# Kernel tuning notes

Hardware: AMD Instinct MI355X
Metric: run time of the kernel (lower is better)

## Reference

```python
import jax, jax.numpy as jnp
import numpy as np

N = 50000
E = 800000
DES, TW, NUMP, CATP = 768, 768, 4, 3
EMB = 384
THIRD = EMB // 3  # 128


def _lin(key, fan_in, fan_out):
    k1, k2 = jax.random.split(key)
    bound = 1.0 / np.sqrt(fan_in)
    W = jax.random.uniform(k1, (fan_in, fan_out), jnp.float32, -bound, bound)
    b = jax.random.uniform(k2, (fan_out,), jnp.float32, -bound, bound)
    return W, b


def setup_inputs() -> dict:
    key = jax.random.key(0)
    ks = jax.random.split(key, 16)
    des = jax.random.normal(ks[0], (N, DES), jnp.float32)
    tweet = jax.random.normal(ks[1], (N, TW), jnp.float32)
    num_prop = jax.random.normal(ks[2], (N, NUMP), jnp.float32)
    cat_prop = jax.random.normal(ks[3], (N, CATP), jnp.float32)
    edge_index = jax.random.randint(ks[4], (2, E), 0, N, jnp.int64)
    W_des, b_des = _lin(ks[5], DES, THIRD)
    W_num, b_num = _lin(ks[6], NUMP, THIRD)
    W_cat, b_cat = _lin(ks[7], CATP, THIRD)
    W_in, b_in = _lin(ks[8], EMB, EMB)
    W_g1, b_g1 = _lin(ks[9], EMB, EMB)
    W_g2, b_g2 = _lin(ks[10], EMB, EMB)
    W_o1, b_o1 = _lin(ks[11], EMB, EMB)
    W_o2, b_o2 = _lin(ks[12], EMB, 2)
    return dict(des=des, tweet=tweet, num_prop=num_prop, cat_prop=cat_prop,
                edge_index=edge_index,
                W_des=W_des, b_des=b_des, W_num=W_num, b_num=b_num,
                W_cat=W_cat, b_cat=b_cat, W_in=W_in, b_in=b_in,
                W_g1=W_g1, b_g1=b_g1, W_g2=W_g2, b_g2=b_g2,
                W_o1=W_o1, b_o1=b_o1, W_o2=W_o2, b_o2=b_o2)


def _leaky(x):
    return jax.nn.leaky_relu(x, 0.01)


def _gcn_conv(x, edge_index, W, b):
    # PyG GCNConv: x' = D^{-1/2} (A + I) D^{-1/2} (x W) + b
    src, dst = edge_index[0], edge_index[1]
    x = x @ W  # [N, out]
    n = x.shape[0]
    deg = jax.ops.segment_sum(jnp.ones(src.shape[0], x.dtype), dst, num_segments=n) + 1.0  # self-loop
    dinv = jax.lax.rsqrt(deg)  # deg >= 1
    norm = dinv[src] * dinv[dst]  # [E]
    msg = x[src] * norm[:, None]  # [E, out] gather
    agg = jax.ops.segment_sum(msg, dst, num_segments=n)  # scatter-add
    agg = agg + x * (dinv * dinv)[:, None]  # self-loop contribution
    return agg + b


def reference(des, tweet, num_prop, cat_prop, edge_index,
              W_des, b_des, W_num, b_num, W_cat, b_cat, W_in, b_in,
              W_g1, b_g1, W_g2, b_g2, W_o1, b_o1, W_o2, b_o2):
    # eval mode: dropout is identity
    d = _leaky(des @ W_des + b_des)
    n = _leaky(num_prop @ W_num + b_num)
    c = _leaky(cat_prop @ W_cat + b_cat)
    x = jnp.concatenate((d, n, c), axis=1)  # [N, EMB]
    x = _leaky(x @ W_in + b_in)
    x = _gcn_conv(x, edge_index, W_g1, b_g1)
    x = _gcn_conv(x, edge_index, W_g2, b_g2)
    x = _leaky(x @ W_o1 + b_o1)
    return x @ W_o2 + b_o2  # [N, 2]
```

## Files before the change

### kernel.cpp

```cpp
#include <hip/hip_runtime.h>
#include <hip/hip_bf16.h>
#include <cstdint>

#define NFEAT 384
#define DESK 768
#define THIRD 128

typedef __bf16 bf16x8 __attribute__((ext_vector_type(8)));
typedef unsigned short u16x8 __attribute__((ext_vector_type(8)));
typedef unsigned short u16x4 __attribute__((ext_vector_type(4)));
typedef float f32x16 __attribute__((ext_vector_type(16)));
typedef _Float16 h16x2 __attribute__((ext_vector_type(2)));

__device__ __forceinline__ float leaky(float x) { return x > 0.f ? x : 0.01f * x; }

__device__ __forceinline__ unsigned short bfhi(float x) {
  unsigned int u = __float_as_uint(x);
  u += 0x7fffu + ((u >> 16) & 1u);
  return (unsigned short)(u >> 16);
}
__device__ __forceinline__ float bf2f(unsigned short h) {
  return __uint_as_float(((unsigned int)h) << 16);
}
__device__ __forceinline__ void bsplit(float x, unsigned short& h,
                                       unsigned short& l) {
  h = bfhi(x);
  l = bfhi(x - bf2f(h));
}

__device__ __forceinline__ int swz(int kb, int row, int ROWS) {
  return (kb * ROWS + (row ^ (kb << 1))) * 8;
}

#define MFMA(a, b, c) __builtin_amdgcn_mfma_f32_32x32x16_bf16(a, b, c, 0, 0, 0)

template <int AFP32, int EPI, int BM, int DBUF>
__global__ __launch_bounds__(256, 2) void mfma_gemm(
    const float* __restrict__ Af, const unsigned short* __restrict__ Ahi,
    const unsigned short* __restrict__ Alo,
    const unsigned short* __restrict__ BThi,
    const unsigned short* __restrict__ BTlo, _Float16* __restrict__ Ch16,
    unsigned short* __restrict__ Chi, unsigned short* __restrict__ Clo,
    const float* __restrict__ bias, int M, int K, int ldc) {
  __shared__ unsigned short AhiL[DBUF + 1][4 * BM * 8];
  __shared__ unsigned short AloL[DBUF + 1][4 * BM * 8];
  __shared__ unsigned short BhiL[DBUF + 1][4 * 128 * 8];
  __shared__ unsigned short BloL[DBUF + 1][4 * 128 * 8];
  const int tid = threadIdx.x;
  const int lane = tid & 63;
  const int w = tid >> 6;
  constexpr int MR = BM / 64;
  const int wm = (w >> 1) * (BM / 2);
  const int wn = (w & 1) * 64;
  const int lm = lane & 31, lk = lane >> 5;

  int bx = blockIdx.x, by = blockIdx.y;
  if (gridDim.y == 3) {
    int lin = by * gridDim.x + bx;
    int ng = gridDim.x >> 3;
    int full = ng * 24;
    if (lin < full) {
      int g = lin / 24, x = lin - g * 24;
      bx = g * 8 + (x & 7);
      by = x >> 3;
    } else {
      int rem = lin - full;
      int mrem = gridDim.x - (ng << 3);
      bx = (ng << 3) + rem % mrem;
      by = rem / mrem;
    }
  }
  const int m_base = bx * BM, n_base = by * 128;

  f32x16 acc[MR][2];
#pragma unroll
  for (int mi = 0; mi < MR; mi++)
#pragma unroll
    for (int nt = 0; nt < 2; nt++)
#pragma unroll
      for (int r = 0; r < 16; r++) acc[mi][nt][r] = 0.f;

  constexpr int AIT_F = BM / 32;
  constexpr int AIT_H = BM / 64;
  float4 pa[3][AIT_F];
  u16x8 pah[3][AIT_H], pal[3][AIT_H];
  u16x8 pbh[3][2], pbl[3][2];

  auto loadA = [&](int kt, int s) {
    if (AFP32) {
#pragma unroll
      for (int it = 0; it < AIT_F; it++) {
        int r = (tid >> 3) + it * 32;
        int gr = m_base + r;
        float4 av = make_float4(0.f, 0.f, 0.f, 0.f);
        if (gr < M) av = *(const float4*)&Af[(size_t)gr * K + kt + (tid & 7) * 4];
        pa[s][it] = av;
      }
    } else {
#pragma unroll
      for (int it = 0; it < AIT_H; it++) {
        int r = (tid >> 2) + it * 64;
        int gr = m_base + r;
        u16x8 vh = {0, 0, 0, 0, 0, 0, 0, 0};
        u16x8 vl = {0, 0, 0, 0, 0, 0, 0, 0};
        if (gr < M) {
          vh = *(const u16x8*)&Ahi[(size_t)gr * K + kt + (tid & 3) * 8];
          vl = *(const u16x8*)&Alo[(size_t)gr * K + kt + (tid & 3) * 8];
        }
        pah[s][it] = vh;
        pal[s][it] = vl;
      }
    }
  };
  auto loadB = [&](int kt, int s) {
#pragma unroll
    for (int it = 0; it < 2; it++) {
      int n = (tid >> 2) + it * 64;
      pbh[s][it] = *(const u16x8*)&BThi[(size_t)(n_base + n) * K + kt + (tid & 3) * 8];
      pbl[s][it] = *(const u16x8*)&BTlo[(size_t)(n_base + n) * K + kt + (tid & 3) * 8];
    }
  };
  auto storeLDS = [&](int s, int b) {
    if (AFP32) {
#pragma unroll
      for (int it = 0; it < AIT_F; it++) {
        int r = (tid >> 3) + it * 32;
        int q = tid & 7;
        float4 av = pa[s][it];
        unsigned short h0, h1, h2, h3, l0, l1, l2, l3;
        bsplit(av.x, h0, l0);
        bsplit(av.y, h1, l1);
        bsplit(av.z, h2, l2);
        bsplit(av.w, h3, l3);
        int base = swz(q >> 1, r, BM) + (q & 1) * 4;
        u16x4 th;
        th.x = h0; th.y = h1; th.z = h2; th.w = h3;
        u16x4 tl;
        tl.x = l0; tl.y = l1; tl.z = l2; tl.w = l3;
        *(u16x4*)&AhiL[b][base] = th;
        *(u16x4*)&AloL[b][base] = tl;
      }
    } else {
#pragma unroll
      for (int it = 0; it < AIT_H; it++) {
        int r = (tid >> 2) + it * 64;
        int kb = tid & 3;
        *(u16x8*)&AhiL[b][swz(kb, r, BM)] = pah[s][it];
        *(u16x8*)&AloL[b][swz(kb, r, BM)] = pal[s][it];
      }
    }
#pragma unroll
    for (int it = 0; it < 2; it++) {
      int n = (tid >> 2) + it * 64;
      int kb = tid & 3;
      *(u16x8*)&BhiL[b][swz(kb, n, 128)] = pbh[s][it];
      *(u16x8*)&BloL[b][swz(kb, n, 128)] = pbl[s][it];
    }
  };
  auto compute = [&](int b) {
#pragma unroll
    for (int ks = 0; ks < 2; ks++) {
      int kb = 2 * ks + lk;
      bf16x8 ah[MR], al[MR];
#pragma unroll
      for (int mi = 0; mi < MR; mi++) {
        ah[mi] = __builtin_bit_cast(
            bf16x8, *(const u16x8*)&AhiL[b][swz(kb, wm + mi * 32 + lm, BM)]);
        al[mi] = __builtin_bit_cast(
            bf16x8, *(const u16x8*)&AloL[b][swz(kb, wm + mi * 32 + lm, BM)]);
      }
      bf16x8 bh0 = __builtin_bit_cast(
          bf16x8, *(const u16x8*)&BhiL[b][swz(kb, wn + lm, 128)]);
      bf16x8 bh1 = __builtin_bit_cast(
          bf16x8, *(const u16x8*)&BhiL[b][swz(kb, wn + 32 + lm, 128)]);
      bf16x8 bl0 = __builtin_bit_cast(
          bf16x8, *(const u16x8*)&BloL[b][swz(kb, wn + lm, 128)]);
      bf16x8 bl1 = __builtin_bit_cast(
          bf16x8, *(const u16x8*)&BloL[b][swz(kb, wn + 32 + lm, 128)]);
#pragma unroll
      for (int mi = 0; mi < MR; mi++) {
        acc[mi][0] = MFMA(ah[mi], bh0, acc[mi][0]);
        acc[mi][1] = MFMA(ah[mi], bh1, acc[mi][1]);
        acc[mi][0] = MFMA(ah[mi], bl0, acc[mi][0]);
        acc[mi][1] = MFMA(ah[mi], bl1, acc[mi][1]);
        acc[mi][0] = MFMA(al[mi], bh0, acc[mi][0]);
        acc[mi][1] = MFMA(al[mi], bh1, acc[mi][1]);
      }
    }
  };

  const int NK = K >> 5;
  loadA(0, 0);
  loadB(0, 0);
  loadA(32, 1);
  loadB(32, 1);
  loadA(64, 2);
  loadB(64, 2);

  if (DBUF) {
    storeLDS(0, 0);
    __syncthreads();
    for (int m6 = 0; m6 < NK / 6; m6++) {
#pragma unroll
      for (int ph = 0; ph < 6; ph++) {
        const int i = m6 * 6 + ph;
        if (i + 1 < NK) storeLDS((ph + 1) % 3, (ph + 1) & 1);
        if (i + 3 < NK) {
          loadA((i + 3) << 5, ph % 3);
          loadB((i + 3) << 5, ph % 3);
        }
        compute(ph & 1);
        __syncthreads();
      }
    }
  } else {
    for (int m3 = 0; m3 < NK / 3; m3++) {
#pragma unroll
      for (int ph = 0; ph < 3; ph++) {
        const int i = m3 * 3 + ph;
        storeLDS(ph, 0);
        __syncthreads();
        if (i + 3 < NK) {
          loadA((i + 3) << 5, ph);
          loadB((i + 3) << 5, ph);
        }
        compute(0);
        __syncthreads();
      }
    }
  }

  const int colb = n_base + wn;
#pragma unroll
  for (int mi = 0; mi < MR; mi++) {
#pragma unroll
    for (int nt = 0; nt < 2; nt++) {
      f32x16 v = acc[mi][nt];
      int col = colb + nt * 32 + lm;
      float bv = (EPI == 0) ? bias[col] : 0.f;
      int rb = m_base + wm + mi * 32 + 4 * lk;
#pragma unroll
      for (int rg = 0; rg < 16; rg++) {
        int row = rb + (rg & 3) + 8 * (rg >> 2);
        if (row < M) {
          float x = v[rg];
          if (EPI == 0) {
            x = leaky(x + bv);
            unsigned short h, l;
            bsplit(x, h, l);
            Chi[(size_t)row * ldc + col] = h;
            Clo[(size_t)row * ldc + col] = l;
          } else {
            Ch16[(size_t)row * ldc + col] = (_Float16)x;
          }
        }
      }
    }
  }
}

__global__ __launch_bounds__(256) void split_transpose_b(
    const float* __restrict__ s0, unsigned short* __restrict__ h0,
    unsigned short* __restrict__ l0, const float* __restrict__ s1,
    unsigned short* __restrict__ h1, unsigned short* __restrict__ l1,
    const float* __restrict__ s2, unsigned short* __restrict__ h2,
    unsigned short* __restrict__ l2) {
  int z = blockIdx.z;
  const float* src = z == 0 ? s0 : (z == 1 ? s1 : s2);
  unsigned short* dsthi = z == 0 ? h0 : (z == 1 ? h1 : h2);
  unsigned short* dstlo = z == 0 ? l0 : (z == 1 ? l1 : l2);
  int R = z == 0 ? 768 : 384;
  int C = z == 0 ? 128 : 384;
  int c0 = blockIdx.x * 32, r0 = blockIdx.y * 32;
  if (c0 >= C || r0 >= R) return;
  __shared__ float tile[32][33];
  int tx = threadIdx.x & 31, ty = threadIdx.x >> 5;
#pragma unroll
  for (int i = 0; i < 4; i++)
    tile[ty + i * 8][tx] = src[(size_t)(r0 + ty + i * 8) * C + c0 + tx];
  __syncthreads();
#pragma unroll
  for (int i = 0; i < 4; i++) {
    int c = c0 + ty + i * 8, r = r0 + tx;
    float v = tile[tx][ty + i * 8];
    unsigned short h, l;
    bsplit(v, h, l);
    dsthi[(size_t)c * R + r] = h;
    dstlo[(size_t)c * R + r] = l;
  }
}

__global__ __launch_bounds__(256) void gemm384(const float* __restrict__ A,
                                               const float* __restrict__ B,
                                               float* __restrict__ C) {
  __shared__ float As[16][68];
  __shared__ float Bs[16][64];
  const int tid = threadIdx.x;
  const int mb = blockIdx.x * 64;
  const int nb = blockIdx.y * 64;
  float acc[4][4] = {};
  const int arow = tid >> 2, akq = tid & 3;
  const int brow = tid >> 4, bc4 = tid & 15;
  const int m0 = (tid >> 4) * 4, n0 = (tid & 15) * 4;
  for (int kk = 0; kk < 384; kk += 16) {
    float4 av = *(const float4*)&A[(mb + arow) * 384 + kk + akq * 4];
    As[akq * 4 + 0][arow] = av.x;
    As[akq * 4 + 1][arow] = av.y;
    As[akq * 4 + 2][arow] = av.z;
    As[akq * 4 + 3][arow] = av.w;
    *(float4*)&Bs[brow][bc4 * 4] =
        *(const float4*)&B[(kk + brow) * 384 + nb + bc4 * 4];
    __syncthreads();
#pragma unroll
    for (int k = 0; k < 16; k++) {
      float4 a4 = *(const float4*)&As[k][m0];
      float4 b4 = *(const float4*)&Bs[k][n0];
      float a[4] = {a4.x, a4.y, a4.z, a4.w};
      float b[4] = {b4.x, b4.y, b4.z, b4.w};
#pragma unroll
      for (int i = 0; i < 4; i++)
#pragma unroll
        for (int j = 0; j < 4; j++) acc[i][j] = fmaf(a[i], b[j], acc[i][j]);
    }
    __syncthreads();
  }
#pragma unroll
  for (int i = 0; i < 4; i++)
#pragma unroll
    for (int j = 0; j < 4; j++)
      C[(mb + m0 + i) * 384 + nb + n0 + j] = acc[i][j];
}

__global__ void uv_kernel(const float* __restrict__ T1,
                          const float* __restrict__ W_o1,
                          const float* __restrict__ b_g1,
                          const float* __restrict__ b_g2,
                          const float* __restrict__ b_o1, float* __restrict__ u,
                          float* __restrict__ v) {
  int j = blockIdx.x * blockDim.x + threadIdx.x;
  if (j < 384) {
    float su = 0.f, sv = 0.f;
    for (int k = 0; k < 384; k++) {
      su = fmaf(T1[k * 384 + j], b_g1[k], su);
      sv = fmaf(W_o1[k * 384 + j], b_g2[k], sv);
    }
    u[j] = su;
    v[j] = sv + b_o1[j];
  }
}

__global__ __launch_bounds__(256) void numcat_kernel(
    const float* __restrict__ num, const float* __restrict__ cat,
    const float* __restrict__ Wn, const float* __restrict__ bn,
    const float* __restrict__ Wc, const float* __restrict__ bc,
    unsigned short* __restrict__ x0hi, unsigned short* __restrict__ x0lo,
    int N) {
  int c = threadIdx.x;
  for (int i = blockIdx.x; i < N; i += gridDim.x) {
    float val;
    if (c < 128) {
      val = bn[c];
      val = fmaf(num[i * 4 + 0], Wn[0 * 128 + c], val);
      val = fmaf(num[i * 4 + 1], Wn[1 * 128 + c], val);
      val = fmaf(num[i * 4 + 2], Wn[2 * 128 + c], val);
      val = fmaf(num[i * 4 + 3], Wn[3 * 128 + c], val);
    } else {
      int cc = c - 128;
      val = bc[cc];
      val = fmaf(cat[i * 3 + 0], Wc[0 * 128 + cc], val);
      val = fmaf(cat[i * 3 + 1], Wc[1 * 128 + cc], val);
      val = fmaf(cat[i * 3 + 2], Wc[2 * 128 + cc], val);
    }
    val = leaky(val);
    unsigned short h, l;
    bsplit(val, h, l);
    size_t o = (size_t)i * NFEAT + 128 + c;
    x0hi[o] = h;
    x0lo[o] = l;
  }
}

__global__ void count_kernel(const int* __restrict__ dst, int* __restrict__ deg,
                             int E) {
  int e = blockIdx.x * blockDim.x + threadIdx.x;
  if (e < E) atomicAdd(&deg[dst[e]], 1);
}

__global__ void scan_reduce(const int* __restrict__ deg,
                            int* __restrict__ partial, int N) {
  __shared__ int sm[512];
  int i = blockIdx.x * 512 + threadIdx.x;
  sm[threadIdx.x] = (i < N) ? deg[i] : 0;
  __syncthreads();
  for (int off = 256; off; off >>= 1) {
    if (threadIdx.x < off) sm[threadIdx.x] += sm[threadIdx.x + off];
    __syncthreads();
  }
  if (threadIdx.x == 0) partial[blockIdx.x] = sm[0];
}

__global__ void scan_top(int* partial, int nb) {
  if (threadIdx.x == 0 && blockIdx.x == 0) {
    int run = 0;
    for (int b = 0; b < nb; b++) {
      int t = partial[b];
      partial[b] = run;
      run += t;
    }
  }
}

__global__ void scan_down(const int* __restrict__ deg,
                          const int* __restrict__ partial,
                          int* __restrict__ offsets, int* __restrict__ cursor,
                          float* __restrict__ dinv, int N, int E) {
  __shared__ int sm[512];
  int t = threadIdx.x;
  int i = blockIdx.x * 512 + t;
  int val = (i < N) ? deg[i] : 0;
  sm[t] = val;
  __syncthreads();
  for (int off = 1; off < 512; off <<= 1) {
    int add = (t >= off) ? sm[t - off] : 0;
    __syncthreads();
    sm[t] += add;
    __syncthreads();
  }
  if (i < N) {
    int ex = partial[blockIdx.x] + sm[t] - val;
    offsets[i] = ex;
    cursor[i] = ex;
    dinv[i] = 1.0f / sqrtf((float)val + 1.0f);
  }
  if (i == 0) offsets[N] = E;
}

__global__ void fill_kernel(const int* __restrict__ src,
                            const int* __restrict__ dst,
                            int* __restrict__ cursor,
                            int* __restrict__ csr_off,
                            float* __restrict__ csr_w,
                            const float* __restrict__ dinv, int E) {
  int e = blockIdx.x * blockDim.x + threadIdx.x;
  if (e < E) {
    int s = src[e], d = dst[e];
    int slot = atomicAdd(&cursor[d], 1);
    csr_off[slot] = s * NFEAT;
    csr_w[slot] = dinv[s] * dinv[d];
  }
}

template <int WRITE_S, int FINAL>
__global__ __launch_bounds__(192) void agg_kernel(
    const _Float16* __restrict__ xin, _Float16* __restrict__ xout,
    const int* __restrict__ offsets, const int* __restrict__ csr_off,
    const float* __restrict__ csr_w, const float* __restrict__ dinv,
    float* __restrict__ sout, const float* __restrict__ svec,
    const float* __restrict__ uvec, const float* __restrict__ vvec,
    const float* __restrict__ W_o2, const float* __restrict__ b_o2,
    float* __restrict__ out, int N) {
  const int t = threadIdx.x;
  const int ff = 2 * t;
  __shared__ int ssrc[192];
  __shared__ float sw[192];
  __shared__ float red[3][2];
  float u0 = 0.f, u1 = 0.f, vc0 = 0.f, vc1 = 0.f;
  float w00 = 0.f, w01 = 0.f, w10 = 0.f, w11 = 0.f, bo0 = 0.f, bo1 = 0.f;
  if (FINAL) {
    u0 = uvec[ff];
    u1 = uvec[ff + 1];
    vc0 = vvec[ff];
    vc1 = vvec[ff + 1];
    w00 = W_o2[ff * 2 + 0];
    w01 = W_o2[ff * 2 + 1];
    w10 = W_o2[(ff + 1) * 2 + 0];
    w11 = W_o2[(ff + 1) * 2 + 1];
    bo0 = b_o2[0];
    bo1 = b_o2[1];
  }
  for (int i = blockIdx.x; i < N; i += gridDim.x) {
    int beg = offsets[i], end = offsets[i + 1];
    float di = dinv[i];
    float dii = di * di;
    h16x2 xs = *(const h16x2*)&xin[(size_t)i * NFEAT + ff];
    float A0x = dii * (float)xs.x, A0y = dii * (float)xs.y;
    float A1x = 0.f, A1y = 0.f, A2x = 0.f, A2y = 0.f, A3x = 0.f, A3y = 0.f;
    float wsum = dii;
    for (int j0 = beg; j0 < end; j0 += 192) {
      int cnt = min(192, end - j0);
      if (t < cnt) {
        ssrc[t] = csr_off[j0 + t];
        sw[t] = csr_w[j0 + t];
      }
      __syncthreads();
      int j = 0;
      for (; j + 8 <= cnt; j += 8) {
        int o0 = ssrc[j + 0], o1 = ssrc[j + 1], o2 = ssrc[j + 2],
            o3 = ssrc[j + 3];
        int o4 = ssrc[j + 4], o5 = ssrc[j + 5], o6 = ssrc[j + 6],
            o7 = ssrc[j + 7];
        float w0 = sw[j + 0], w1 = sw[j + 1], w2 = sw[j + 2], w3 = sw[j + 3];
        float w4 = sw[j + 4], w5 = sw[j + 5], w6 = sw[j + 6], w7 = sw[j + 7];
        h16x2 v0 = *(const h16x2*)&xin[o0 + ff];
        h16x2 v1 = *(const h16x2*)&xin[o1 + ff];
        h16x2 v2 = *(const h16x2*)&xin[o2 + ff];
        h16x2 v3 = *(const h16x2*)&xin[o3 + ff];
        h16x2 v4 = *(const h16x2*)&xin[o4 + ff];
        h16x2 v5 = *(const h16x2*)&xin[o5 + ff];
        h16x2 v6 = *(const h16x2*)&xin[o6 + ff];
        h16x2 v7 = *(const h16x2*)&xin[o7 + ff];
        A0x = fmaf(w0, (float)v0.x, A0x);
        A0y = fmaf(w0, (float)v0.y, A0y);
        A1x = fmaf(w1, (float)v1.x, A1x);
        A1y = fmaf(w1, (float)v1.y, A1y);
        A2x = fmaf(w2, (float)v2.x, A2x);
        A2y = fmaf(w2, (float)v2.y, A2y);
        A3x = fmaf(w3, (float)v3.x, A3x);
        A3y = fmaf(w3, (float)v3.y, A3y);
        A0x = fmaf(w4, (float)v4.x, A0x);
        A0y = fmaf(w4, (float)v4.y, A0y);
        A1x = fmaf(w5, (float)v5.x, A1x);
        A1y = fmaf(w5, (float)v5.y, A1y);
        A2x = fmaf(w6, (float)v6.x, A2x);
        A2y = fmaf(w6, (float)v6.y, A2y);
        A3x = fmaf(w7, (float)v7.x, A3x);
        A3y = fmaf(w7, (float)v7.y, A3y);
        if (WRITE_S) wsum += ((w0 + w1) + (w2 + w3)) + ((w4 + w5) + (w6 + w7));
      }
      for (; j < cnt; j++) {
        float wj = sw[j];
        h16x2 vj = *(const h16x2*)&xin[ssrc[j] + ff];
        A0x = fmaf(wj, (float)vj.x, A0x);
        A0y = fmaf(wj, (float)vj.y, A0y);
        if (WRITE_S) wsum += wj;
      }
      __syncthreads();
    }
    float ax = (A0x + A1x) + (A2x + A3x);
    float ay = (A0y + A1y) + (A2y + A3y);
    if (!FINAL) {
      h16x2 r;
      r.x = (_Float16)ax;
      r.y = (_Float16)ay;
      *(h16x2*)&xout[(size_t)i * NFEAT + ff] = r;
      if (WRITE_S && t == 0) sout[i] = wsum;
    } else {
      float si = svec[i];
      float q0 = leaky(ax + si * u0 + vc0);
      float q1 = leaky(ay + si * u1 + vc1);
      float c0 = q0 * w00 + q1 * w10;
      float c1 = q0 * w01 + q1 * w11;
#pragma unroll
      for (int off2 = 32; off2; off2 >>= 1) {
        c0 += __shfl_down(c0, off2, 64);
        c1 += __shfl_down(c1, off2, 64);
      }
      int wid = t >> 6, lane2 = t & 63;
      if (lane2 == 0) {
        red[wid][0] = c0;
        red[wid][1] = c1;
      }
      __syncthreads();
      if (t == 0) {
        out[i * 2 + 0] = red[0][0] + red[1][0] + red[2][0] + bo0;
        out[i * 2 + 1] = red[0][1] + red[1][1] + red[2][1] + bo1;
      }
    }
  }
}

extern "C" void kernel_launch(void* const* d_in, const int* in_sizes, int n_in,
                              void* d_out, int out_size, void* d_ws,
                              size_t ws_size, hipStream_t stream) {
  const float* des = (const float*)d_in[0];
  const float* num_prop = (const float*)d_in[2];
  const float* cat_prop = (const float*)d_in[3];
  const int* edge = (const int*)d_in[4];
  const float* W_des = (const float*)d_in[5];
  const float* b_des = (const float*)d_in[6];
  const float* W_num = (const float*)d_in[7];
  const float* b_num = (const float*)d_in[8];
  const float* W_cat = (const float*)d_in[9];
  const float* b_cat = (const float*)d_in[10];
  const float* W_in = (const float*)d_in[11];
  const float* b_in = (const float*)d_in[12];
  const float* W_g1 = (const float*)d_in[13];
  const float* b_g1 = (const float*)d_in[14];
  const float* W_g2 = (const float*)d_in[15];
  const float* b_g2 = (const float*)d_in[16];
  const float* W_o1 = (const float*)d_in[17];
  const float* b_o1 = (const float*)d_in[18];
  const float* W_o2 = (const float*)d_in[19];
  const float* b_o2 = (const float*)d_in[20];
  float* out = (float*)d_out;

  const int N = in_sizes[0] / DESK;
  const int E = in_sizes[4] / 2;
  const int* esrc = edge;
  const int* edst = edge + E;

  char* ws = (char*)d_ws;
  size_t off = 0;
  auto alloc = [&](size_t n) {
    off = (off + 255) & ~(size_t)255;
    size_t o = off;
    off += n;
    return o;
  };
  float* bufA = (float*)(ws + alloc((size_t)N * NFEAT * 4));
  float* bufB = (float*)(ws + alloc((size_t)N * NFEAT * 4));
  int* deg = (int*)(ws + alloc((size_t)N * 4));
  int* offsets = (int*)(ws + alloc((size_t)(N + 1) * 4));
  int* cursor = (int*)(ws + alloc((size_t)N * 4));
  int* partial = (int*)(ws + alloc(1024 * 4));
  float* dinv = (float*)(ws + alloc((size_t)N * 4));
  float* svec = (float*)(ws + alloc((size_t)N * 4));
  int* csr_off = (int*)(ws + alloc((size_t)E * 4));
  float* csr_w = (float*)(ws + alloc((size_t)E * 4));
  float* T1 = (float*)(ws + alloc(384 * 384 * 4));
  float* Mmat = (float*)(ws + alloc(384 * 384 * 4));
  float* uvec = (float*)(ws + alloc(384 * 4));
  float* vvec = (float*)(ws + alloc(384 * 4));
  unsigned short* WdThi = (unsigned short*)(ws + alloc(768 * 128 * 2));
  unsigned short* WdTlo = (unsigned short*)(ws + alloc(768 * 128 * 2));
  unsigned short* WiThi = (unsigned short*)(ws + alloc(384 * 384 * 2));
  unsigned short* WiTlo = (unsigned short*)(ws + alloc(384 * 384 * 2));
  unsigned short* MmThi = (unsigned short*)(ws + alloc(384 * 384 * 2));
  unsigned short* MmTlo = (unsigned short*)(ws + alloc(384 * 384 * 2));
  (void)ws_size;
  (void)n_in;
  (void)out_size;

  unsigned short* x0hi = (unsigned short*)bufA;
  unsigned short* x0lo = x0hi + (size_t)N * NFEAT;
  unsigned short* x1hi = (unsigned short*)bufB;
  unsigned short* x1lo = x1hi + (size_t)N * NFEAT;
  _Float16* yb = (_Float16*)bufA;
  _Float16* w1 = (_Float16*)bufB;

  hipMemsetAsync(deg, 0, (size_t)N * 4, stream);

  dim3 g6(6, 6);
  gemm384<<<g6, 256, 0, stream>>>(W_g2, W_o1, T1);
  gemm384<<<g6, 256, 0, stream>>>(W_g1, T1, Mmat);
  uv_kernel<<<2, 256, 0, stream>>>(T1, W_o1, b_g1, b_g2, b_o1, uvec, vvec);
  split_transpose_b<<<dim3(12, 24, 3), 256, 0, stream>>>(
      W_des, WdThi, WdTlo, W_in, WiThi, WiTlo, Mmat, MmThi, MmTlo);

  const int MT = (N + 127) / 128;
  const int MT64 = (N + 63) / 64;
  mfma_gemm<1, 0, 64, 0><<<dim3(MT64, 1), 256, 0, stream>>>(
      des, nullptr, nullptr, WdThi, WdTlo, nullptr, x0hi, x0lo, b_des, N, DESK,
      NFEAT);
  numcat_kernel<<<1024, 256, 0, stream>>>(num_prop, cat_prop, W_num, b_num,
                                          W_cat, b_cat, x0hi, x0lo, N);
  mfma_gemm<0, 0, 128, 1><<<dim3(MT, 3), 256, 0, stream>>>(
      nullptr, x0hi, x0lo, WiThi, WiTlo, nullptr, x1hi, x1lo, b_in, N, NFEAT,
      NFEAT);
  mfma_gemm<0, 1, 128, 1><<<dim3(MT, 3), 256, 0, stream>>>(
      nullptr, x1hi, x1lo, MmThi, MmTlo, yb, nullptr, nullptr, nullptr, N,
      NFEAT, NFEAT);

  const int EB = (E + 255) / 256;
  count_kernel<<<EB, 256, 0, stream>>>(edst, deg, E);
  const int NB = (N + 511) / 512;
  scan_reduce<<<NB, 512, 0, stream>>>(deg, partial, N);
  scan_top<<<1, 64, 0, stream>>>(partial, NB);
  scan_down<<<NB, 512, 0, stream>>>(deg, partial, offsets, cursor, dinv, N, E);
  fill_kernel<<<EB, 256, 0, stream>>>(esrc, edst, cursor, csr_off, csr_w, dinv,
                                      E);

  agg_kernel<1, 0><<<4096, 192, 0, stream>>>(
      yb, w1, offsets, csr_off, csr_w, dinv, svec, nullptr, nullptr, nullptr,
      nullptr, nullptr, nullptr, N);
  agg_kernel<0, 1><<<4096, 192, 0, stream>>>(
      w1, nullptr, offsets, csr_off, csr_w, dinv, nullptr, svec, uvec, vvec,
      W_o2, b_o2, out, N);
}
```

Measured before the change: 912.1 us.

## Slice feature matrix into 48-column panels for cache-local SpMM aggregation

The GEMM epilogue now writes the fp16 feature matrix as 8 column panels of 48 features each, and the aggregation kernels assign each block to one panel, with 24-thread teams handling one node each. Each gathered neighbour row is then a small contiguous chunk inside a panel of roughly 4.8 MB, which should keep the random gathers cache-resident and cut traffic to HBM. The final layer's per-node dot product is now split across panels, so output is initialised with the bias and accumulated with atomics. In exchange, edge indices and weights are read straight from global memory by every team, and the atomics make the floating-point summation order nondeterministic.

```diff
diff --git a/kernel.cpp b/kernel.cpp
--- a/kernel.cpp
+++ b/kernel.cpp
@@ -239,6 +239,8 @@
       int col = colb + nt * 32 + lm;
       float bv = (EPI == 0) ? bias[col] : 0.f;
       int rb = m_base + wm + mi * 32 + 4 * lk;
+      int p = col / 48;
+      size_t pbase = (size_t)p * M * 48 + (col - p * 48);
 #pragma unroll
       for (int rg = 0; rg < 16; rg++) {
         int row = rb + (rg & 3) + 8 * (rg >> 2);
@@ -251,7 +253,7 @@
             Chi[(size_t)row * ldc + col] = h;
             Clo[(size_t)row * ldc + col] = l;
           } else {
-            Ch16[(size_t)row * ldc + col] = (_Float16)x;
+            Ch16[pbase + (size_t)row * 48] = (_Float16)x;
           }
         }
       }
@@ -445,126 +447,146 @@
   if (e < E) {
     int s = src[e], d = dst[e];
     int slot = atomicAdd(&cursor[d], 1);
-    csr_off[slot] = s * NFEAT;
+    csr_off[slot] = s * 48;
     csr_w[slot] = dinv[s] * dinv[d];
   }
 }
 
+__global__ void init_out(const float* __restrict__ b_o2,
+                         float* __restrict__ out, int N) {
+  int i = blockIdx.x * blockDim.x + threadIdx.x;
+  if (i < N) {
+    out[2 * i + 0] = b_o2[0];
+    out[2 * i + 1] = b_o2[1];
+  }
+}
+
 template <int WRITE_S, int FINAL>
-__global__ __launch_bounds__(192) void agg_kernel(
+__global__ __launch_bounds__(192) void agg_slice(
     const _Float16* __restrict__ xin, _Float16* __restrict__ xout,
     const int* __restrict__ offsets, const int* __restrict__ csr_off,
     const float* __restrict__ csr_w, const float* __restrict__ dinv,
     float* __restrict__ sout, const float* __restrict__ svec,
     const float* __restrict__ uvec, const float* __restrict__ vvec,
-    const float* __restrict__ W_o2, const float* __restrict__ b_o2,
-    float* __restrict__ out, int N) {
+    const float* __restrict__ W_o2, float* __restrict__ out, int N) {
   const int t = threadIdx.x;
-  const int ff = 2 * t;
-  __shared__ int ssrc[192];
-  __shared__ float sw[192];
-  __shared__ float red[3][2];
+  const int team = t / 24;
+  const int l = t - team * 24;
+  const int slice = blockIdx.x & 7;
+  const int sb = blockIdx.x >> 3;
+  const int teams_per_slice = (gridDim.x >> 3) * 8;
+  const _Float16* xp = xin + (size_t)slice * N * 48;
+  const int t0 = sb * 8 + team;
+  __shared__ float red[192][2];
+
   float u0 = 0.f, u1 = 0.f, vc0 = 0.f, vc1 = 0.f;
-  float w00 = 0.f, w01 = 0.f, w10 = 0.f, w11 = 0.f, bo0 = 0.f, bo1 = 0.f;
+  float w00 = 0.f, w01 = 0.f, w10 = 0.f, w11 = 0.f;
   if (FINAL) {
-    u0 = uvec[ff];
-    u1 = uvec[ff + 1];
-    vc0 = vvec[ff];
-    vc1 = vvec[ff + 1];
-    w00 = W_o2[ff * 2 + 0];
-    w01 = W_o2[ff * 2 + 1];
-    w10 = W_o2[(ff + 1) * 2 + 0];
-    w11 = W_o2[(ff + 1) * 2 + 1];
-    bo0 = b_o2[0];
-    bo1 = b_o2[1];
-  }
-  for (int i = blockIdx.x; i < N; i += gridDim.x) {
+    const int f = slice * 48 + 2 * l;
+    u0 = uvec[f];
+    u1 = uvec[f + 1];
+    vc0 = vvec[f];
+    vc1 = vvec[f + 1];
+    w00 = W_o2[f * 2 + 0];
+    w01 = W_o2[f * 2 + 1];
+    w10 = W_o2[(f + 1) * 2 + 0];
+    w11 = W_o2[(f + 1) * 2 + 1];
+  }
+
+  auto dorow = [&](int i, float& ax, float& ay, float& wsum) {
     int beg = offsets[i], end = offsets[i + 1];
     float di = dinv[i];
     float dii = di * di;
-    h16x2 xs = *(const h16x2*)&xin[(size_t)i * NFEAT + ff];
+    h16x2 xs = *(const h16x2*)&xp[(size_t)i * 48 + 2 * l];
     float A0x = dii * (float)xs.x, A0y = dii * (float)xs.y;
     float A1x = 0.f, A1y = 0.f, A2x = 0.f, A2y = 0.f, A3x = 0.f, A3y = 0.f;
-    float wsum = dii;
-    for (int j0 = beg; j0 < end; j0 += 192) {
-      int cnt = min(192, end - j0);
-      if (t < cnt) {
-        ssrc[t] = csr_off[j0 + t];
-        sw[t] = csr_w[j0 + t];
-      }
+    wsum = dii;
+    int j = beg;
+    for (; j + 8 <= end; j += 8) {
+      int o0 = csr_off[j + 0], o1 = csr_off[j + 1], o2 = csr_off[j + 2],
+          o3 = csr_off[j + 3];
+      int o4 = csr_off[j + 4], o5 = csr_off[j + 5], o6 = csr_off[j + 6],
+          o7 = csr_off[j + 7];
+      float w0 = csr_w[j + 0], w1 = csr_w[j + 1], w2 = csr_w[j + 2],
+            w3 = csr_w[j + 3];
+      float w4 = csr_w[j + 4], w5 = csr_w[j + 5], w6 = csr_w[j + 6],
+            w7 = csr_w[j + 7];
+      h16x2 v0 = *(const h16x2*)&xp[o0 + 2 * l];
+      h16x2 v1 = *(const h16x2*)&xp[o1 + 2 * l];
+      h16x2 v2 = *(const h16x2*)&xp[o2 + 2 * l];
+      h16x2 v3 = *(const h16x2*)&xp[o3 + 2 * l];
+      h16x2 v4 = *(const h16x2*)&xp[o4 + 2 * l];
+      h16x2 v5 = *(const h16x2*)&xp[o5 + 2 * l];
+      h16x2 v6 = *(const h16x2*)&xp[o6 + 2 * l];
+      h16x2 v7 = *(const h16x2*)&xp[o7 + 2 * l];
+      A0x = fmaf(w0, (float)v0.x, A0x);
+      A0y = fmaf(w0, (float)v0.y, A0y);
+      A1x = fmaf(w1, (float)v1.x, A1x);
+      A1y = fmaf(w1, (float)v1.y, A1y);
+      A2x = fmaf(w2, (float)v2.x, A2x);
+      A2y = fmaf(w2, (float)v2.y, A2y);
+      A3x = fmaf(w3, (float)v3.x, A3x);
+      A3y = fmaf(w3, (float)v3.y, A3y);
+      A0x = fmaf(w4, (float)v4.x, A0x);
+      A0y = fmaf(w4, (float)v4.y, A0y);
+      A1x = fmaf(w5, (float)v5.x, A1x);
+      A1y = fmaf(w5, (float)v5.y, A1y);
+      A2x = fmaf(w6, (float)v6.x, A2x);
+      A2y = fmaf(w6, (float)v6.y, A2y);
+      A3x = fmaf(w7, (float)v7.x, A3x);
+      A3y = fmaf(w7, (float)v7.y, A3y);
+      if (WRITE_S) wsum += ((w0 + w1) + (w2 + w3)) + ((w4 + w5) + (w6 + w7));
+    }
+    for (; j < end; j++) {
+      float wj = csr_w[j];
+      h16x2 vj = *(const h16x2*)&xp[csr_off[j] + 2 * l];
+      A0x = fmaf(wj, (float)vj.x, A0x);
+      A0y = fmaf(wj, (float)vj.y, A0y);
+      if (WRITE_S) wsum += wj;
+    }
+    ax = (A0x + A1x) + (A2x + A3x);
+    ay = (A0y + A1y) + (A2y + A3y);
+  };
+
+  if (FINAL) {
+    const int iters = (N + teams_per_slice - 1) / teams_per_slice;
+    for (int it = 0; it < iters; it++) {
+      const int i = t0 + it * teams_per_slice;
+      float c0 = 0.f, c1 = 0.f;
+      if (i < N) {
+        float ax, ay, wsum;
+        dorow(i, ax, ay, wsum);
+        float si = svec[i];
+        float q0 = leaky(ax + si * u0 + vc0);
+        float q1 = leaky(ay + si * u1 + vc1);
+        c0 = q0 * w00 + q1 * w10;
+        c1 = q0 * w01 + q1 * w11;
+      }
+      red[t][0] = c0;
+      red[t][1] = c1;
       __syncthreads();
-      int j = 0;
-      for (; j + 8 <= cnt; j += 8) {
-        int o0 = ssrc[j + 0], o1 = ssrc[j + 1], o2 = ssrc[j + 2],
-            o3 = ssrc[j + 3];
-        int o4 = ssrc[j + 4], o5 = ssrc[j + 5], o6 = ssrc[j + 6],
-            o7 = ssrc[j + 7];
-        float w0 = sw[j + 0], w1 = sw[j + 1], w2 = sw[j + 2], w3 = sw[j + 3];
-        float w4 = sw[j + 4], w5 = sw[j + 5], w6 = sw[j + 6], w7 = sw[j + 7];
-        h16x2 v0 = *(const h16x2*)&xin[o0 + ff];
-        h16x2 v1 = *(const h16x2*)&xin[o1 + ff];
-        h16x2 v2 = *(const h16x2*)&xin[o2 + ff];
-        h16x2 v3 = *(const h16x2*)&xin[o3 + ff];
-        h16x2 v4 = *(const h16x2*)&xin[o4 + ff];
-        h16x2 v5 = *(const h16x2*)&xin[o5 + ff];
-        h16x2 v6 = *(const h16x2*)&xin[o6 + ff];
-        h16x2 v7 = *(const h16x2*)&xin[o7 + ff];
-        A0x = fmaf(w0, (float)v0.x, A0x);
-        A0y = fmaf(w0, (float)v0.y, A0y);
-        A1x = fmaf(w1, (float)v1.x, A1x);
-        A1y = fmaf(w1, (float)v1.y, A1y);
-        A2x = fmaf(w2, (float)v2.x, A2x);
-        A2y = fmaf(w2, (float)v2.y, A2y);
-        A3x = fmaf(w3, (float)v3.x, A3x);
-        A3y = fmaf(w3, (float)v3.y, A3y);
-        A0x = fmaf(w4, (float)v4.x, A0x);
-        A0y = fmaf(w4, (float)v4.y, A0y);
-        A1x = fmaf(w5, (float)v5.x, A1x);
-        A1y = fmaf(w5, (float)v5.y, A1y);
-        A2x = fmaf(w6, (float)v6.x, A2x);
-        A2y = fmaf(w6, (float)v6.y, A2y);
-        A3x = fmaf(w7, (float)v7.x, A3x);
-        A3y = fmaf(w7, (float)v7.y, A3y);
-        if (WRITE_S) wsum += ((w0 + w1) + (w2 + w3)) + ((w4 + w5) + (w6 + w7));
-      }
-      for (; j < cnt; j++) {
-        float wj = sw[j];
-        h16x2 vj = *(const h16x2*)&xin[ssrc[j] + ff];
-        A0x = fmaf(wj, (float)vj.x, A0x);
-        A0y = fmaf(wj, (float)vj.y, A0y);
-        if (WRITE_S) wsum += wj;
+      if (t < 16) {
+        int tm = t >> 1, c = t & 1;
+        int i2 = sb * 8 + tm + it * teams_per_slice;
+        if (i2 < N) {
+          float s = 0.f;
+#pragma unroll
+          for (int k = 0; k < 24; k++) s += red[tm * 24 + k][c];
+          atomicAdd(&out[i2 * 2 + c], s);
+        }
       }
       __syncthreads();
     }
-    float ax = (A0x + A1x) + (A2x + A3x);
-    float ay = (A0y + A1y) + (A2y + A3y);
-    if (!FINAL) {
+  } else {
+    _Float16* op = xout + (size_t)slice * N * 48;
+    for (int i = t0; i < N; i += teams_per_slice) {
+      float ax, ay, wsum;
+      dorow(i, ax, ay, wsum);
       h16x2 r;
       r.x = (_Float16)ax;
       r.y = (_Float16)ay;
-      *(h16x2*)&xout[(size_t)i * NFEAT + ff] = r;
-      if (WRITE_S && t == 0) sout[i] = wsum;
-    } else {
-      float si = svec[i];
-      float q0 = leaky(ax + si * u0 + vc0);
-      float q1 = leaky(ay + si * u1 + vc1);
-      float c0 = q0 * w00 + q1 * w10;
-      float c1 = q0 * w01 + q1 * w11;
-#pragma unroll
-      for (int off2 = 32; off2; off2 >>= 1) {
-        c0 += __shfl_down(c0, off2, 64);
-        c1 += __shfl_down(c1, off2, 64);
-      }
-      int wid = t >> 6, lane2 = t & 63;
-      if (lane2 == 0) {
-        red[wid][0] = c0;
-        red[wid][1] = c1;
-      }
-      __syncthreads();
-      if (t == 0) {
-        out[i * 2 + 0] = red[0][0] + red[1][0] + red[2][0] + bo0;
-        out[i * 2 + 1] = red[0][1] + red[1][1] + red[2][1] + bo1;
-      }
+      *(h16x2*)&op[(size_t)i * 48 + 2 * l] = r;
+      if (WRITE_S && slice == 0 && l == 0) sout[i] = wsum;
     }
   }
 }
@@ -669,11 +691,13 @@
   scan_down<<<NB, 512, 0, stream>>>(deg, partial, offsets, cursor, dinv, N, E);
   fill_kernel<<<EB, 256, 0, stream>>>(esrc, edst, cursor, csr_off, csr_w, dinv,
                                       E);
-
-  agg_kernel<1, 0><<<4096, 192, 0, stream>>>(
+  init_out<<<(N + 255) / 256, 256, 0, stream>>>(b_o2, out, N);
+
+  const int NBS = 512;
+  agg_slice<1, 0><<<8 * NBS, 192, 0, stream>>>(
       yb, w1, offsets, csr_off, csr_w, dinv, svec, nullptr, nullptr, nullptr,
-      nullptr, nullptr, nullptr, N);
-  agg_kernel<0, 1><<<4096, 192, 0, stream>>>(
+      nullptr, nullptr, N);
+  agg_slice<0, 1><<<8 * NBS, 192, 0, stream>>>(
       w1, nullptr, offsets, csr_off, csr_w, dinv, nullptr, svec, uvec, vvec,
-      W_o2, b_o2, out, N);
-}
+      W_o2, out, N);
+}
```

New measurement: 1.023 ms. +12.1%, slower.
